# Optimization experiments

Hardware: AMD Instinct MI355X
Metric: run time of the kernel (lower is better)

The kernel has to match this reference:

```python
import jax, jax.numpy as jnp
import numpy as np

B, D_IN, UNITS = 8192, 4096, 4096

def setup_inputs() -> dict:
    key = jax.random.key(0)
    k1, k2 = jax.random.split(key)
    x = jax.random.normal(k1, (B, D_IN), dtype=jnp.float32)
    w = jax.random.normal(k2, (D_IN, UNITS), dtype=jnp.float32)
    b = jnp.zeros((UNITS,), dtype=jnp.float32)
    return {"x": x, "w": w, "b": b}

def reference(x, w, b):
    # Bipolar dense: sign-binarize the weights, full-precision matmul, bias, relu.
    weights = jnp.sign(w)  # values in {-1, 0, +1}; matches tf.math.sign
    out = jnp.matmul(x, weights) + b  # [B, UNITS]
    return jax.nn.relu(out)
```

## Files before the change

kernel.cpp:

```cpp
#include <hip/hip_runtime.h>
#include <hip/hip_bf16.h>
#include <stdint.h>

#define M_DIM 8192
#define N_DIM 4096
#define K_DIM 4096

typedef __attribute__((ext_vector_type(4)))  int   int4v;
typedef __attribute__((ext_vector_type(16))) int   int16v;
typedef __attribute__((ext_vector_type(4)))  float floatx4;

__global__ __launch_bounds__(256) void quant_x_kernel(const float* __restrict__ x,
                                                      signed char* __restrict__ xq,
                                                      float* __restrict__ xs) {
    const int row = blockIdx.x;
    const int tid = threadIdx.x;
    const int wave = tid >> 6, lane = tid & 63;
    const float4* xr = (const float4*)(x + (size_t)row * K_DIM);

    float4 v[4];
    float m = 0.f;
    #pragma unroll
    for (int j = 0; j < 4; ++j) {
        v[j] = xr[j * 256 + tid];
        m = fmaxf(m, fmaxf(fmaxf(fabsf(v[j].x), fabsf(v[j].y)),
                           fmaxf(fabsf(v[j].z), fabsf(v[j].w))));
    }
    #pragma unroll
    for (int off = 32; off >= 1; off >>= 1) m = fmaxf(m, __shfl_down(m, off));
    __shared__ float wm[4];
    if (lane == 0) wm[wave] = m;
    __syncthreads();
    const float M = fmaxf(fmaxf(wm[0], wm[1]), fmaxf(wm[2], wm[3]));
    const float inv = M > 0.f ? 127.f / M : 0.f;
    if (tid == 0) xs[row] = M > 0.f ? M / 127.f : 0.f;

    char4* xo = (char4*)(xq + (size_t)row * K_DIM);
    #pragma unroll
    for (int j = 0; j < 4; ++j) {
        char4 q;
        q.x = (signed char)__float2int_rn(v[j].x * inv);
        q.y = (signed char)__float2int_rn(v[j].y * inv);
        q.z = (signed char)__float2int_rn(v[j].z * inv);
        q.w = (signed char)__float2int_rn(v[j].w * inv);
        xo[j * 256 + tid] = q;
    }
}

__global__ __launch_bounds__(256) void cvt_w_kernel(const float* __restrict__ w,
                                                    signed char* __restrict__ wT) {
    __shared__ signed char tile[64][68];
    const int t  = threadIdx.x;
    const int k0 = blockIdx.y * 64;
    const int n0 = blockIdx.x * 64;
    #pragma unroll
    for (int p = 0; p < 4; ++p) {
        int kk = p * 16 + (t >> 4);
        int nn = (t & 15) * 4;
        float4 v = *reinterpret_cast<const float4*>(&w[(size_t)(k0 + kk) * N_DIM + n0 + nn]);
        tile[kk][nn + 0] = v.x > 0.f ? 1 : (v.x < 0.f ? -1 : 0);
        tile[kk][nn + 1] = v.y > 0.f ? 1 : (v.y < 0.f ? -1 : 0);
        tile[kk][nn + 2] = v.z > 0.f ? 1 : (v.z < 0.f ? -1 : 0);
        tile[kk][nn + 3] = v.w > 0.f ? 1 : (v.w < 0.f ? -1 : 0);
    }
    __syncthreads();
    const int r = t >> 2;
    const int c = (t & 3) * 16;
    int4v o;
    signed char* op = (signed char*)&o;
    #pragma unroll
    for (int j = 0; j < 16; ++j) op[j] = tile[c + j][r];
    *reinterpret_cast<int4v*>(&wT[(size_t)(n0 + r) * K_DIM + k0 + c]) = o;
}

#define BM 256
#define BN 256
#define BK 64
#define NT (K_DIM / BK)

#define GLD(gsrc, ldst) __builtin_amdgcn_global_load_lds( \
    (const __attribute__((address_space(1))) unsigned int*)(gsrc), \
    (__attribute__((address_space(3))) unsigned int*)(ldst), 16, 0, 0)

__global__ __launch_bounds__(512, 2) void gemm_i8_kernel(
    const signed char* __restrict__ A,
    const signed char* __restrict__ BT,
    const float* __restrict__ xsc,
    const float* __restrict__ bias,
    float* __restrict__ C)
{
    __shared__ signed char As[2][2][128 * 64];
    __shared__ signed char Bs[2][2][128 * 64];

    const int tid  = threadIdx.x;
    const int wave = tid >> 6;
    const int lane = tid & 63;
    const int wm   = wave >> 2;
    const int wn   = wave & 3;
    const int bh   = wn >> 1;
    const int brow0 = (wn & 1) * 64;

    const int bid  = blockIdx.x;
    const int sbid = (bid & 7) * 64 + (bid >> 3);
    const int tn   = sbid & 15;
    const int tm   = sbid >> 4;
    const int bm   = tm * BM;
    const int bn   = tn * BN;

    const int srow = tid >> 2;
    const int scol = ((tid & 3) ^ ((tid >> 3) & 3)) * 16;

    const int laneRow = (lane & 31) * 64;
    const int fsw = ((lane >> 1) & 3) << 4;
    const int colX0 = (((lane >> 5) << 4) | 0)  ^ fsw;
    const int colX1 = (((lane >> 5) << 4) | 32) ^ fsw;

    int16v acc[4][2] = {};

#define STAGE_HALF(G, R0, KOFS, LDST) do { \
    GLD((G) + (size_t)((R0) + srow) * K_DIM + (KOFS) + scol, (LDST) + wave * 1024); \
  } while (0)

    STAGE_HALF(BT, bn,        0, Bs[0][0]);
    STAGE_HALF(BT, bn + 128,  0, Bs[0][1]);
    STAGE_HALF(A,  bm,        0, As[0][0]);
    STAGE_HALF(A,  bm + 128,  0, As[0][1]);
    STAGE_HALF(BT, bn,       BK, Bs[1][0]);
    STAGE_HALF(BT, bn + 128, BK, Bs[1][1]);
    asm volatile("s_waitcnt vmcnt(2)" ::: "memory");
    __builtin_amdgcn_s_barrier();

    int4v a[2][2];
    int4v a2[2][2];
    int4v b[2][2];

    for (int t = 0; t < NT; ++t) {
        const int buf = t & 1;
        const char* Ar = (const char*)As[buf][wm];
        const char* Br = (const char*)Bs[buf][bh];
        const int kA = (t + 1 < NT ? t + 1 : NT - 1) * BK;
        const int kB = (t + 2 < NT ? t + 2 : NT - 1) * BK;

        a[0][0] = *(const int4v*)(Ar + (0*32)*64 + laneRow + colX0);
        b[0][0] = *(const int4v*)(Br + (brow0 + 0*32)*64 + laneRow + colX0);
        b[0][1] = *(const int4v*)(Br + (brow0 + 0*32)*64 + laneRow + colX1);
        b[1][0] = *(const int4v*)(Br + (brow0 + 1*32)*64 + laneRow + colX0);
        b[1][1] = *(const int4v*)(Br + (brow0 + 1*32)*64 + laneRow + colX1);
        a[0][1] = *(const int4v*)(Ar + (0*32)*64 + laneRow + colX1);
        a[1][0] = *(const int4v*)(Ar + (1*32)*64 + laneRow + colX0);
        a[1][1] = *(const int4v*)(Ar + (1*32)*64 + laneRow + colX1);
        STAGE_HALF(A, bm,       kA, As[buf ^ 1][0]);
        STAGE_HALF(A, bm + 128, kA, As[buf ^ 1][1]);
        __builtin_amdgcn_s_setprio(1);
        #pragma unroll
        for (int mb = 0; mb < 2; ++mb)
            #pragma unroll
            for (int nb = 0; nb < 2; ++nb)
                #pragma unroll
                for (int ks = 0; ks < 2; ++ks)
                    acc[mb][nb] = __builtin_amdgcn_mfma_i32_32x32x32_i8(
                        a[mb][ks], b[nb][ks], acc[mb][nb], 0, 0, 0);
        __builtin_amdgcn_s_setprio(0);
        __builtin_amdgcn_s_barrier();

        a2[0][0] = *(const int4v*)(Ar + (2*32)*64 + laneRow + colX0);
        a2[0][1] = *(const int4v*)(Ar + (2*32)*64 + laneRow + colX1);
        a2[1][0] = *(const int4v*)(Ar + (3*32)*64 + laneRow + colX0);
        a2[1][1] = *(const int4v*)(Ar + (3*32)*64 + laneRow + colX1);
        asm volatile("" ::: "memory");
        STAGE_HALF(BT, bn,       kB, Bs[buf][0]);
        STAGE_HALF(BT, bn + 128, kB, Bs[buf][1]);
        __builtin_amdgcn_s_setprio(1);
        #pragma unroll
        for (int mb = 0; mb < 2; ++mb)
            #pragma unroll
            for (int nb = 0; nb < 2; ++nb)
                #pragma unroll
                for (int ks = 0; ks < 2; ++ks)
                    acc[2 + mb][nb] = __builtin_amdgcn_mfma_i32_32x32x32_i8(
                        a2[mb][ks], b[nb][ks], acc[2 + mb][nb], 0, 0, 0);
        __builtin_amdgcn_s_setprio(0);
        asm volatile("s_waitcnt vmcnt(2)" ::: "memory");
        __builtin_amdgcn_s_barrier();
    }

    #pragma unroll
    for (int mb = 0; mb < 4; ++mb) {
        const int row0 = bm + wm * 128 + mb * 32 + 4 * (lane >> 5);
        float4 s[4];
        #pragma unroll
        for (int q = 0; q < 4; ++q)
            s[q] = *reinterpret_cast<const float4*>(&xsc[row0 + 8 * q]);
        #pragma unroll
        for (int nb = 0; nb < 2; ++nb) {
            const int col = bn + wn * 64 + nb * 32 + (lane & 31);
            const float bvv = bias[col];
            #pragma unroll
            for (int q = 0; q < 4; ++q)
                #pragma unroll
                for (int j = 0; j < 4; ++j) {
                    const int row = row0 + 8 * q + j;
                    float v = (float)acc[mb][nb][q * 4 + j] * ((const float*)&s[q])[j] + bvv;
                    C[(size_t)row * N_DIM + col] = v > 0.f ? v : 0.f;
                }
        }
    }
}

__global__ void naive_kernel(const float* __restrict__ x, const float* __restrict__ w,
                             const float* __restrict__ b, float* __restrict__ out) {
    __shared__ float xs[16][16];
    __shared__ float ws[16][17];
    const int row = blockIdx.y * 16 + threadIdx.y;
    const int col = blockIdx.x * 16 + threadIdx.x;
    float acc = 0.f;
    for (int k0 = 0; k0 < K_DIM; k0 += 16) {
        xs[threadIdx.y][threadIdx.x] = x[(size_t)row * K_DIM + k0 + threadIdx.x];
        float wv = w[(size_t)(k0 + threadIdx.y) * N_DIM + col];
        ws[threadIdx.y][threadIdx.x] = wv > 0.f ? 1.f : (wv < 0.f ? -1.f : 0.f);
        __syncthreads();
        #pragma unroll
        for (int kk = 0; kk < 16; ++kk) acc += xs[threadIdx.y][kk] * ws[kk][threadIdx.x];
        __syncthreads();
    }
    float v = acc + b[col];
    out[(size_t)row * N_DIM + col] = v > 0.f ? v : 0.f;
}

extern "C" void kernel_launch(void* const* d_in, const int* in_sizes, int n_in,
                              void* d_out, int out_size, void* d_ws, size_t ws_size,
                              hipStream_t stream) {
    const float* x = (const float*)d_in[0];
    const float* w = (const float*)d_in[1];
    const float* b = (const float*)d_in[2];
    float* out = (float*)d_out;

    const size_t xq_bytes = (size_t)M_DIM * K_DIM;
    const size_t wT_bytes = (size_t)K_DIM * N_DIM;
    const size_t xs_bytes = (size_t)M_DIM * sizeof(float);

    if (ws_size >= xq_bytes + wT_bytes + xs_bytes) {
        signed char* xq = (signed char*)d_ws;
        signed char* wT = (signed char*)((char*)d_ws + xq_bytes);
        float*       xs = (float*)((char*)d_ws + xq_bytes + wT_bytes);
        quant_x_kernel<<<M_DIM, 256, 0, stream>>>(x, xq, xs);
        cvt_w_kernel<<<dim3(N_DIM / 64, K_DIM / 64), 256, 0, stream>>>(w, wT);
        gemm_i8_kernel<<<(M_DIM / BM) * (N_DIM / BN), 512, 0, stream>>>(xq, wT, xs, b, out);
    } else {
        naive_kernel<<<dim3(N_DIM / 16, M_DIM / 16), dim3(16, 16), 0, stream>>>(x, w, b, out);
    }
}
```

Before: 200.0 us.

## Double K tile to 128 and simplify double-buffered staging schedule

Raises the GEMM K-tile from 64 to 128 so each iteration issues 16 MFMAs per accumulator group, halving the number of barriers and loop iterations. It also replaces the staggered A/B split staging with a plain double buffer: both operands for the next tile are prefetched, then the loop waits for all loads at the end. LDS per block grows to 128 KB, which likely allows only one 512-thread block per CU instead of two and reduces latency hiding. The swizzle is widened to 8 chunks to fit the 128-byte rows.

```diff
diff --git a/kernel.cpp b/kernel.cpp
--- a/kernel.cpp
+++ b/kernel.cpp
@@ -8,7 +8,6 @@
 
 typedef __attribute__((ext_vector_type(4)))  int   int4v;
 typedef __attribute__((ext_vector_type(16))) int   int16v;
-typedef __attribute__((ext_vector_type(4)))  float floatx4;
 
 __global__ __launch_bounds__(256) void quant_x_kernel(const float* __restrict__ x,
                                                       signed char* __restrict__ xq,
@@ -75,7 +74,7 @@
 
 #define BM 256
 #define BN 256
-#define BK 64
+#define BK 128
 #define NT (K_DIM / BK)
 
 #define GLD(gsrc, ldst) __builtin_amdgcn_global_load_lds( \
@@ -89,16 +88,14 @@
     const float* __restrict__ bias,
     float* __restrict__ C)
 {
-    __shared__ signed char As[2][2][128 * 64];
-    __shared__ signed char Bs[2][2][128 * 64];
+    __shared__ signed char As[2][256 * 128];
+    __shared__ signed char Bs[2][256 * 128];
 
     const int tid  = threadIdx.x;
     const int wave = tid >> 6;
     const int lane = tid & 63;
     const int wm   = wave >> 2;
     const int wn   = wave & 3;
-    const int bh   = wn >> 1;
-    const int brow0 = (wn & 1) * 64;
 
     const int bid  = blockIdx.x;
     const int sbid = (bid & 7) * 64 + (bid >> 3);
@@ -107,80 +104,87 @@
     const int bm   = tm * BM;
     const int bn   = tn * BN;
 
-    const int srow = tid >> 2;
-    const int scol = ((tid & 3) ^ ((tid >> 3) & 3)) * 16;
-
-    const int laneRow = (lane & 31) * 64;
-    const int fsw = ((lane >> 1) & 3) << 4;
-    const int colX0 = (((lane >> 5) << 4) | 0)  ^ fsw;
-    const int colX1 = (((lane >> 5) << 4) | 32) ^ fsw;
+    const int srow = tid >> 3;
+    const int scol = (((tid & 7) ^ ((tid >> 4) & 7)) << 4);
+
+    const int laneRow = (lane & 31) * 128;
+    const int fsw  = ((lane >> 1) & 7) << 4;
+    const int hb   = (lane >> 5) << 4;
+    const int colX0 = (  0 + hb) ^ fsw;
+    const int colX1 = ( 32 + hb) ^ fsw;
+    const int colX2 = ( 64 + hb) ^ fsw;
+    const int colX3 = ( 96 + hb) ^ fsw;
+    const int Abase = wm * 128 * 128;
+    const int Bbase = wn * 64 * 128;
 
     int16v acc[4][2] = {};
 
-#define STAGE_HALF(G, R0, KOFS, LDST) do { \
-    GLD((G) + (size_t)((R0) + srow) * K_DIM + (KOFS) + scol, (LDST) + wave * 1024); \
+#define STAGE_T(G, R0, KOFS, LDSLOT) do { \
+    _Pragma("unroll") \
+    for (int s = 0; s < 4; ++s) \
+        GLD((G) + (size_t)((R0) + s * 64 + srow) * K_DIM + (KOFS) + scol, \
+            (LDSLOT) + s * 8192 + wave * 1024); \
   } while (0)
 
-    STAGE_HALF(BT, bn,        0, Bs[0][0]);
-    STAGE_HALF(BT, bn + 128,  0, Bs[0][1]);
-    STAGE_HALF(A,  bm,        0, As[0][0]);
-    STAGE_HALF(A,  bm + 128,  0, As[0][1]);
-    STAGE_HALF(BT, bn,       BK, Bs[1][0]);
-    STAGE_HALF(BT, bn + 128, BK, Bs[1][1]);
-    asm volatile("s_waitcnt vmcnt(2)" ::: "memory");
+    STAGE_T(A,  bm, 0, As[0]);
+    STAGE_T(BT, bn, 0, Bs[0]);
+    asm volatile("s_waitcnt vmcnt(0)" ::: "memory");
     __builtin_amdgcn_s_barrier();
 
-    int4v a[2][2];
-    int4v a2[2][2];
-    int4v b[2][2];
+    int4v b[2][4];
+    int4v aE[2][4];
+    int4v aL[2][4];
 
     for (int t = 0; t < NT; ++t) {
-        const int buf = t & 1;
-        const char* Ar = (const char*)As[buf][wm];
-        const char* Br = (const char*)Bs[buf][bh];
-        const int kA = (t + 1 < NT ? t + 1 : NT - 1) * BK;
-        const int kB = (t + 2 < NT ? t + 2 : NT - 1) * BK;
-
-        a[0][0] = *(const int4v*)(Ar + (0*32)*64 + laneRow + colX0);
-        b[0][0] = *(const int4v*)(Br + (brow0 + 0*32)*64 + laneRow + colX0);
-        b[0][1] = *(const int4v*)(Br + (brow0 + 0*32)*64 + laneRow + colX1);
-        b[1][0] = *(const int4v*)(Br + (brow0 + 1*32)*64 + laneRow + colX0);
-        b[1][1] = *(const int4v*)(Br + (brow0 + 1*32)*64 + laneRow + colX1);
-        a[0][1] = *(const int4v*)(Ar + (0*32)*64 + laneRow + colX1);
-        a[1][0] = *(const int4v*)(Ar + (1*32)*64 + laneRow + colX0);
-        a[1][1] = *(const int4v*)(Ar + (1*32)*64 + laneRow + colX1);
-        STAGE_HALF(A, bm,       kA, As[buf ^ 1][0]);
-        STAGE_HALF(A, bm + 128, kA, As[buf ^ 1][1]);
+        const int rd = t & 1;
+        const char* Ar = (const char*)As[rd];
+        const char* Br = (const char*)Bs[rd];
+        const int kS = (t + 1 < NT ? t + 1 : NT - 1) * BK;
+
+        #pragma unroll
+        for (int ks = 0; ks < 4; ++ks) {
+            b[0][ks] = *(const int4v*)(Br + Bbase + 0 * 4096 + laneRow +
+                                       (ks == 0 ? colX0 : ks == 1 ? colX1 : ks == 2 ? colX2 : colX3));
+            b[1][ks] = *(const int4v*)(Br + Bbase + 1 * 4096 + laneRow +
+                                       (ks == 0 ? colX0 : ks == 1 ? colX1 : ks == 2 ? colX2 : colX3));
+        }
+        #pragma unroll
+        for (int mb = 0; mb < 2; ++mb)
+            #pragma unroll
+            for (int ks = 0; ks < 4; ++ks)
+                aE[mb][ks] = *(const int4v*)(Ar + Abase + mb * 4096 + laneRow +
+                                       (ks == 0 ? colX0 : ks == 1 ? colX1 : ks == 2 ? colX2 : colX3));
+
+        STAGE_T(A,  bm, kS, As[rd ^ 1]);
+        STAGE_T(BT, bn, kS, Bs[rd ^ 1]);
+
         __builtin_amdgcn_s_setprio(1);
         #pragma unroll
         for (int mb = 0; mb < 2; ++mb)
             #pragma unroll
             for (int nb = 0; nb < 2; ++nb)
                 #pragma unroll
-                for (int ks = 0; ks < 2; ++ks)
+                for (int ks = 0; ks < 4; ++ks)
                     acc[mb][nb] = __builtin_amdgcn_mfma_i32_32x32x32_i8(
-                        a[mb][ks], b[nb][ks], acc[mb][nb], 0, 0, 0);
-        __builtin_amdgcn_s_setprio(0);
-        __builtin_amdgcn_s_barrier();
-
-        a2[0][0] = *(const int4v*)(Ar + (2*32)*64 + laneRow + colX0);
-        a2[0][1] = *(const int4v*)(Ar + (2*32)*64 + laneRow + colX1);
-        a2[1][0] = *(const int4v*)(Ar + (3*32)*64 + laneRow + colX0);
-        a2[1][1] = *(const int4v*)(Ar + (3*32)*64 + laneRow + colX1);
-        asm volatile("" ::: "memory");
-        STAGE_HALF(BT, bn,       kB, Bs[buf][0]);
-        STAGE_HALF(BT, bn + 128, kB, Bs[buf][1]);
-        __builtin_amdgcn_s_setprio(1);
+                        aE[mb][ks], b[nb][ks], acc[mb][nb], 0, 0, 0);
+
+        #pragma unroll
+        for (int mb = 0; mb < 2; ++mb)
+            #pragma unroll
+            for (int ks = 0; ks < 4; ++ks)
+                aL[mb][ks] = *(const int4v*)(Ar + Abase + (2 + mb) * 4096 + laneRow +
+                                       (ks == 0 ? colX0 : ks == 1 ? colX1 : ks == 2 ? colX2 : colX3));
         #pragma unroll
         for (int mb = 0; mb < 2; ++mb)
             #pragma unroll
             for (int nb = 0; nb < 2; ++nb)
                 #pragma unroll
-                for (int ks = 0; ks < 2; ++ks)
+                for (int ks = 0; ks < 4; ++ks)
                     acc[2 + mb][nb] = __builtin_amdgcn_mfma_i32_32x32x32_i8(
-                        a2[mb][ks], b[nb][ks], acc[2 + mb][nb], 0, 0, 0);
+                        aL[mb][ks], b[nb][ks], acc[2 + mb][nb], 0, 0, 0);
         __builtin_amdgcn_s_setprio(0);
-        asm volatile("s_waitcnt vmcnt(2)" ::: "memory");
+
+        asm volatile("s_waitcnt vmcnt(0)" ::: "memory");
         __builtin_amdgcn_s_barrier();
     }
 
```

After: 186.3 us. 6.8% less time.
